# Kernel tuning notes

Hardware: AMD Instinct MI355X
Metric: run time of the kernel (lower is better)

## Reference

```python
import jax, jax.numpy as jnp
import numpy as np

B, S, D = 4, 4096, 64

def setup_inputs() -> dict:
    key = jax.random.key(0)
    ks = jax.random.split(key, 6)
    mk = lambda k: jax.random.normal(k, (B, S, D), dtype=jnp.float32)
    return {
        "q_re": mk(ks[0]), "q_im": mk(ks[1]),
        "k_re": mk(ks[2]), "k_im": mk(ks[3]),
        "v_re": mk(ks[4]), "v_im": mk(ks[5]),
    }

def reference(q_re, q_im, k_re, k_im, v_re, v_im):
    # Complex QK^T (no conjugate, matching torch.bmm on complex tensors):
    # (qr + i qi)(kr + i ki)^T -> re = qr kr^T - qi ki^T ; im = qr ki^T + qi kr^T
    d_k = q_re.shape[-1]
    scale = 1.0 / jnp.sqrt(jnp.asarray(d_k, dtype=q_re.dtype))
    s_re = (jnp.einsum('bqd,bkd->bqk', q_re, k_re)
            - jnp.einsum('bqd,bkd->bqk', q_im, k_im)) * scale
    s_im = (jnp.einsum('bqd,bkd->bqk', q_re, k_im)
            + jnp.einsum('bqd,bkd->bqk', q_im, k_re)) * scale
    # softmax over |scores| along key axis; weights are real (imag part is 0)
    w = jax.nn.softmax(jnp.sqrt(s_re * s_re + s_im * s_im), axis=-1)  # [B,S,S]
    # CVDropout is identity in eval mode. Output = real_weights @ complex_values
    o_re = jnp.einsum('bqk,bkd->bqd', w, v_re)
    o_im = jnp.einsum('bqk,bkd->bqd', w, v_im)
    return jnp.stack([o_re, o_im], axis=0)  # [2, B, S, D] (real, imag)
```

## Files before the change

kernel.cpp:

```cpp
#include <hip/hip_runtime.h>
#include <stdint.h>

#define B_    4
#define S_    4096
#define D_    64
#define QBLK  128
#define NELEM (B_ * S_ * D_)
#define BS_   (B_ * S_)

typedef __attribute__((ext_vector_type(8))) short bf16x8;
typedef __attribute__((ext_vector_type(4))) short bf16x4;
typedef __attribute__((ext_vector_type(4))) float f32x4;
typedef __attribute__((ext_vector_type(4))) int   i32x4;
typedef __attribute__((ext_vector_type(4))) unsigned u32x4;
typedef __attribute__((ext_vector_type(4))) _Float16 f16x4;

#define MFMA(a, b, c) __builtin_amdgcn_mfma_f32_16x16x32_bf16(a, b, c, 0, 0, 0)
#define VMWAIT(n) asm volatile("s_waitcnt vmcnt(" #n ")" ::: "memory")
#define BARRIER() do { asm volatile("" ::: "memory"); __builtin_amdgcn_s_barrier(); asm volatile("" ::: "memory"); } while (0)
#define LGKM_FENCE() do { asm volatile("s_waitcnt lgkmcnt(0)" ::: "memory"); __builtin_amdgcn_sched_barrier(0); } while (0)

__device__ __forceinline__ short f2bf(float x) {
    unsigned u = __builtin_bit_cast(unsigned, x);
    u += 0x7FFFu + ((u >> 16) & 1u);
    return (short)(u >> 16);
}

__device__ __forceinline__ unsigned cvtpk(float lo, float hi) {
    unsigned r;
    asm("v_cvt_pk_bf16_f32 %0, %1, %2" : "=v"(r) : "v"(lo), "v"(hi));
    return r;
}

__device__ __forceinline__ void async16(const short* g, short* l) {
    __builtin_amdgcn_global_load_lds(
        (const __attribute__((address_space(1))) unsigned int*)g,
        (__attribute__((address_space(3))) unsigned int*)l, 16, 0, 0);
}

__global__ __launch_bounds__(256)
void prepass_kernel(const float* __restrict__ q_re, const float* __restrict__ q_im,
                    const float* __restrict__ k_re, const float* __restrict__ k_im,
                    const float* __restrict__ v_re, const float* __restrict__ v_im,
                    short* __restrict__ ws) {
    const int bidx = blockIdx.x;
    const int tid  = threadIdx.x;
    if (bidx < 4096) {
        const int idx = bidx * 256 + tid;
        const int tn  = idx >> 18;
        const int e4  = idx & ((1 << 18) - 1);
        const float* s = (tn == 0 ? q_re : tn == 1 ? q_im : tn == 2 ? k_re : k_im)
                         + (size_t)e4 * 4;
        const float sc = (tn < 2) ? 0.125f : 1.0f;
        f32x4 x = *(const f32x4*)s;
        bf16x4 v;
#pragma unroll
        for (int c = 0; c < 4; ++c) v[c] = f2bf(x[c] * sc);
        *(bf16x4*)(ws + (size_t)tn * NELEM + (size_t)e4 * 4) = v;
    } else {
        __shared__ short tile[64][72];
        const int tb   = bidx - 4096;
        const int sb   = tb & 63;
        const int b    = (tb >> 6) & 3;
        const int comp = tb >> 8;
        const float* src = comp ? v_im : v_re;
        short* dst = ws + (size_t)(4 + comp) * NELEM;
#pragma unroll
        for (int i = 0; i < 4; ++i) {
            const int slot = i * 256 + tid;
            const int s  = slot >> 4;
            const int d4 = slot & 15;
            f32x4 x = *(const f32x4*)(src + (((size_t)b * S_) + sb * 64 + s) * D_ + d4 * 4);
#pragma unroll
            for (int c = 0; c < 4; ++c) tile[d4 * 4 + c][s] = f2bf(x[c]);
        }
        __syncthreads();
#pragma unroll
        for (int i = 0; i < 2; ++i) {
            const int slot = i * 256 + tid;
            const int d = slot >> 3;
            const int m = slot & 7;
            const int a = m >> 2, hh = m & 3;
            bf16x8 v;
#pragma unroll
            for (int j = 0; j < 8; ++j)
                v[j] = tile[d][a * 32 + hh * 4 + ((j >> 2) << 4) + (j & 3)];
            *(bf16x8*)(dst + ((size_t)b * 64 + d) * S_ + sb * 64 + m * 8) = v;
        }
    }
}

template<int SPLIT, typename OT>
__global__ __launch_bounds__(256, 2)
void cv_attn_main(const short* __restrict__ wsb,
                  float* __restrict__ out,
                  OT* __restrict__ opart,
                  float* __restrict__ ml)
{
    __shared__ __align__(16) short smem[2 * 8192];

    const int tid  = threadIdx.x;
    const int lane = tid & 63;
    const int wv   = tid >> 6;
    const int l15  = lane & 15;
    const int h    = lane >> 4;

    int bid = blockIdx.x;
    const int nwg = B_ * 32 * SPLIT;
    bid = (bid & 7) * (nwg >> 3) + (bid >> 3);
    const int qb = bid & 31;
    const int sp = (bid >> 5) % SPLIT;
    const int b  = bid / (32 * SPLIT);

    const short* qr = wsb;
    const short* qi = wsb + (size_t)NELEM;
    const short* kr = wsb + 2 * (size_t)NELEM;
    const short* ki = wsb + 3 * (size_t)NELEM;
    const short* vT = wsb + 4 * (size_t)NELEM;

    const short* p0 = smem + l15 * 64 + ((h ^ (l15 & 7)) << 3);
    const short* p1 = smem + l15 * 64 + (((h ^ 4) ^ (l15 & 7)) << 3);

    bf16x8 fqr[2][2], fqi[2][2];
#pragma unroll
    for (int g = 0; g < 2; ++g) {
        const int qrow = qb * QBLK + wv * 32 + g * 16 + l15;
        const size_t qoff = ((size_t)b * S_ + qrow) * D_;
#pragma unroll
        for (int dh = 0; dh < 2; ++dh) {
            fqr[g][dh] = *(const bf16x8*)(qr + qoff + dh * 32 + h * 8);
            fqi[g][dh] = *(const bf16x8*)(qi + qoff + dh * 32 + h * 8);
        }
    }

    f32x4 o_re[2][4], o_im[2][4];
#pragma unroll
    for (int g = 0; g < 2; ++g)
#pragma unroll
        for (int i = 0; i < 4; ++i) {
            o_re[g][i] = (f32x4){0.f, 0.f, 0.f, 0.f};
            o_im[g][i] = (f32x4){0.f, 0.f, 0.f, 0.f};
        }
    float l_run[2] = {0.f, 0.f};
    const float L2E = 1.44269504088896f;
    const float NM  = -16.0f * L2E;

    const int srcg = (lane & 7) ^ (lane >> 3);
    const int kRow = wv * 8 + (lane >> 3);
    constexpr int TPB = (S_ / 32) / SPLIT;

    auto stage = [&](int t, int DST) {
        const int kb = (sp * TPB + t) * 32;
        const size_t koff = ((size_t)b * S_ + kb + kRow) * 64 + (srcg << 3);
        async16(kr + koff, smem + DST + wv * 512);
        async16(ki + koff, smem + DST + 2048 + wv * 512);
#pragma unroll
        for (int i = 0; i < 2; ++i) {
            const int d = (wv + 4 * i) * 8 + (lane >> 3);
            const short* src = vT + ((srcg >> 2) ? (size_t)NELEM : (size_t)0)
                               + ((size_t)b * 64 + d) * S_ + kb + (srcg & 3) * 8;
            async16(src, smem + DST + 4096 + wv * 512 + i * 2048);
        }
    };

    auto body = [&](int t, int CUR, int OTH) {
        VMWAIT(0);
        LGKM_FENCE();
        BARRIER();
        if (t + 1 < TPB) stage(t + 1, OTH);

        f32x4 s_re[2][2], s_im[2][2];
#pragma unroll
        for (int g = 0; g < 2; ++g)
#pragma unroll
            for (int c = 0; c < 2; ++c) {
                s_re[g][c] = (f32x4){0.f, 0.f, 0.f, 0.f};
                s_im[g][c] = (f32x4){0.f, 0.f, 0.f, 0.f};
            }
        __builtin_amdgcn_s_setprio(1);
#pragma unroll
        for (int c = 0; c < 2; ++c) {
            bf16x8 a0 = *(const bf16x8*)(p0 + CUR + c * 1024);
            bf16x8 a1 = *(const bf16x8*)(p1 + CUR + c * 1024);
            bf16x8 b0 = *(const bf16x8*)(p0 + CUR + 2048 + c * 1024);
            bf16x8 b1 = *(const bf16x8*)(p1 + CUR + 2048 + c * 1024);
#pragma unroll
            for (int g = 0; g < 2; ++g) {
                i32x4 n0 = __builtin_bit_cast(i32x4, fqi[g][0]) ^ (int)0x80008000;
                i32x4 n1 = __builtin_bit_cast(i32x4, fqi[g][1]) ^ (int)0x80008000;
                bf16x8 fn0 = __builtin_bit_cast(bf16x8, n0);
                bf16x8 fn1 = __builtin_bit_cast(bf16x8, n1);
                s_re[g][c] = MFMA(a0, fqr[g][0], s_re[g][c]);
                s_re[g][c] = MFMA(a1, fqr[g][1], s_re[g][c]);
                s_re[g][c] = MFMA(b0, fn0,       s_re[g][c]);
                s_re[g][c] = MFMA(b1, fn1,       s_re[g][c]);
                s_im[g][c] = MFMA(b0, fqr[g][0], s_im[g][c]);
                s_im[g][c] = MFMA(b1, fqr[g][1], s_im[g][c]);
                s_im[g][c] = MFMA(a0, fqi[g][0], s_im[g][c]);
                s_im[g][c] = MFMA(a1, fqi[g][1], s_im[g][c]);
            }
        }
        __builtin_amdgcn_s_setprio(0);

        bf16x8 pb[2];
#pragma unroll
        for (int g = 0; g < 2; ++g) {
#pragma unroll
            for (int c = 0; c < 2; ++c) {
                f32x4 gm = s_re[g][c] * s_re[g][c] + s_im[g][c] * s_im[g][c];
#pragma unroll
                for (int r = 0; r < 4; ++r) {
                    const float mg = __builtin_amdgcn_sqrtf(gm[r]);
                    s_im[g][c][r] = __builtin_amdgcn_exp2f(__builtin_fmaf(mg, L2E, NM));
                }
            }
            f32x4 ps = s_im[g][0] + s_im[g][1];
            l_run[g] += (ps[0] + ps[1]) + (ps[2] + ps[3]);
            u32x4 w;
            w[0] = cvtpk(s_im[g][0][0], s_im[g][0][1]);
            w[1] = cvtpk(s_im[g][0][2], s_im[g][0][3]);
            w[2] = cvtpk(s_im[g][1][0], s_im[g][1][1]);
            w[3] = cvtpk(s_im[g][1][2], s_im[g][1][3]);
            pb[g] = __builtin_bit_cast(bf16x8, w);
        }

        __builtin_amdgcn_s_setprio(1);
#pragma unroll
        for (int dc = 0; dc < 4; ++dc) {
            bf16x8 av = *(const bf16x8*)(p0 + CUR + 4096 + dc * 1024);
            bf16x8 ai = *(const bf16x8*)(p1 + CUR + 4096 + dc * 1024);
#pragma unroll
            for (int g = 0; g < 2; ++g) {
                o_re[g][dc] = MFMA(av, pb[g], o_re[g][dc]);
                o_im[g][dc] = MFMA(ai, pb[g], o_im[g][dc]);
            }
        }
        __builtin_amdgcn_s_setprio(0);
    };

    stage(0, 0);
    for (int tt = 0; tt < TPB; tt += 2) {
        body(tt,     0,    8192);
        body(tt + 1, 8192, 0);
    }

    float inv[2];
    float lt[2];
#pragma unroll
    for (int g = 0; g < 2; ++g) {
        float l = l_run[g];
        l += __shfl_xor(l, 16);
        l += __shfl_xor(l, 32);
        lt[g]  = l;
        inv[g] = 1.0f / l;
    }

    float* ol = (float*)smem;

    OT* dst_re;
    OT* dst_im;
    if constexpr (SPLIT == 1) {
        dst_re = (OT*)out + ((size_t)b * S_ + qb * QBLK) * D_;
        dst_im = dst_re + (size_t)NELEM;
    } else {
        const size_t qo = ((size_t)b * S_ + qb * QBLK) * D_;
        dst_re = opart + ((size_t)sp * 2 + 0) * NELEM + qo;
        dst_im = opart + ((size_t)sp * 2 + 1) * NELEM + qo;
    }

    auto store_comp = [&](const f32x4 (&oc)[2][4], OT* og) {
#pragma unroll
        for (int half = 0; half < 2; ++half) {
            __syncthreads();
            if ((wv >> 1) == half) {
                const int wl = wv & 1;
#pragma unroll
                for (int g = 0; g < 2; ++g)
#pragma unroll
                    for (int dc = 0; dc < 4; ++dc)
#pragma unroll
                        for (int r = 0; r < 4; ++r)
                            ol[(wl * 32 + g * 16 + l15) * 65 + dc * 16 + h * 4 + r]
                                = oc[g][dc][r] * inv[g];
            }
            __syncthreads();
#pragma unroll
            for (int i = 0; i < 4; ++i) {
                const int slot = i * 256 + tid;
                const int row  = slot >> 4;
                const int c4   = slot & 15;
                f32x4 v;
#pragma unroll
                for (int j = 0; j < 4; ++j) v[j] = ol[row * 65 + c4 * 4 + j];
                if constexpr (sizeof(OT) == 4) {
                    *(f32x4*)((float*)og + (size_t)(half * 64 + row) * D_ + c4 * 4) = v;
                } else {
                    f16x4 hv;
#pragma unroll
                    for (int j = 0; j < 4; ++j) hv[j] = (_Float16)v[j];
                    *(f16x4*)((_Float16*)og + (size_t)(half * 64 + row) * D_ + c4 * 4) = hv;
                }
            }
        }
    };
    store_comp(o_re, dst_re);
    store_comp(o_im, dst_im);

    if constexpr (SPLIT > 1) {
        if (lane < 16) {
#pragma unroll
            for (int g = 0; g < 2; ++g) {
                const int row = qb * QBLK + wv * 32 + g * 16 + lane;
                ml[(size_t)sp * BS_ + (size_t)b * S_ + row] = lt[g];
            }
        }
    }
}

template<int SPLIT, typename OT>
__global__ __launch_bounds__(256)
void cv_attn_combine(const OT* __restrict__ opart, const float* __restrict__ ml,
                     float* __restrict__ out) {
    const int idx  = blockIdx.x * 256 + threadIdx.x;
    const int d4   = idx & 15;
    const int rest = idx >> 4;
    const int row  = rest & (BS_ - 1);
    const int comp = rest >> 14;
    float W = 0.f;
    f32x4 acc = (f32x4){0.f, 0.f, 0.f, 0.f};
#pragma unroll
    for (int s = 0; s < SPLIT; ++s) {
        const float l = ml[(size_t)s * BS_ + row];
        W += l;
        const OT* op = opart + ((size_t)(s * 2 + comp)) * NELEM + (size_t)row * D_ + d4 * 4;
        f32x4 o;
        if constexpr (sizeof(OT) == 4) {
            o = *(const f32x4*)op;
        } else {
            f16x4 hv = *(const f16x4*)op;
#pragma unroll
            for (int j = 0; j < 4; ++j) o[j] = (float)hv[j];
        }
        acc += o * l;
    }
    acc *= (1.0f / W);
    *(f32x4*)(out + (size_t)comp * NELEM + (size_t)row * D_ + d4 * 4) = acc;
}

__global__ __launch_bounds__(256, 1)
void cv_attn_legacy(const float* __restrict__ q_re, const float* __restrict__ q_im,
                    const float* __restrict__ k_re, const float* __restrict__ k_im,
                    const float* __restrict__ v_re, const float* __restrict__ v_im,
                    float* __restrict__ out)
{
    __shared__ __align__(16) short smem[4 * 64 * D_];
    short* kr_s = smem;
    short* ki_s = smem + 4096;
    short* vr_s = smem + 8192;
    short* vi_s = smem + 12288;

    const int tid  = threadIdx.x;
    const int lane = tid & 63;
    const int wv   = tid >> 6;
    const int l15  = lane & 15;
    const int h    = lane >> 4;

    const int b  = blockIdx.x >> 6;
    const int qb = blockIdx.x & 63;
    const size_t boff = (size_t)b * S_ * D_;

    const int qrow = qb * 64 + wv * 16 + l15;
    const float* qrp = q_re + boff + (size_t)qrow * D_;
    const float* qip = q_im + boff + (size_t)qrow * D_;
    bf16x8 fqr[2], fqi[2], fqn[2];
#pragma unroll
    for (int dh = 0; dh < 2; ++dh) {
        const int d0 = dh * 32 + h * 8;
        f32x4 a0 = *(const f32x4*)(qrp + d0);
        f32x4 a1 = *(const f32x4*)(qrp + d0 + 4);
        f32x4 b0 = *(const f32x4*)(qip + d0);
        f32x4 b1 = *(const f32x4*)(qip + d0 + 4);
#pragma unroll
        for (int j = 0; j < 4; ++j) {
            fqr[dh][j] = f2bf(a0[j]); fqr[dh][j + 4] = f2bf(a1[j]);
            fqi[dh][j] = f2bf(b0[j]); fqi[dh][j + 4] = f2bf(b1[j]);
            fqn[dh][j] = f2bf(-b0[j]); fqn[dh][j + 4] = f2bf(-b1[j]);
        }
    }

    f32x4 o_re[4], o_im[4];
#pragma unroll
    for (int i = 0; i < 4; ++i) {
        o_re[i] = (f32x4){0.f, 0.f, 0.f, 0.f};
        o_im[i] = (f32x4){0.f, 0.f, 0.f, 0.f};
    }
    float m_run = -1e30f, l_run = 0.f;
    const float SC = 0.125f * 1.44269504088896f;

    for (int t = 0; t < S_ / 64; ++t) {
        const int kb = t * 64;
#pragma unroll
        for (int a = 0; a < 2; ++a) {
            const float* src = (a ? k_im : k_re) + boff;
            short* dst = a ? ki_s : kr_s;
#pragma unroll
            for (int i = 0; i < 2; ++i) {
                const int slot = i * 256 + tid;
                const int row  = slot >> 3;
                const int cb   = slot & 7;
                const float* p = src + (size_t)(kb + row) * D_ + cb * 8;
                f32x4 x0 = *(const f32x4*)p;
                f32x4 x1 = *(const f32x4*)(p + 4);
                bf16x8 v;
#pragma unroll
                for (int j = 0; j < 4; ++j) { v[j] = f2bf(x0[j]); v[j + 4] = f2bf(x1[j]); }
                *(bf16x8*)(dst + row * 64 + ((cb ^ (row & 7)) << 3)) = v;
            }
        }
#pragma unroll
        for (int a = 0; a < 2; ++a) {
            const float* src = (a ? v_im : v_re) + boff;
            short* dst = a ? vi_s : vr_s;
#pragma unroll
            for (int i = 0; i < 4; ++i) {
                const int slot = i * 256 + tid;
                const int k  = slot >> 4;
                const int d4 = slot & 15;
                f32x4 x = *(const f32x4*)(src + (size_t)(kb + k) * D_ + d4 * 4);
#pragma unroll
                for (int c = 0; c < 4; ++c) {
                    const int d = d4 * 4 + c;
                    dst[d * 64 + (((k >> 2) ^ (d & 15)) << 2) + (k & 3)] = f2bf(x[c]);
                }
            }
        }
        __syncthreads();

        f32x4 s_re[4], s_im[4];
#pragma unroll
        for (int c = 0; c < 4; ++c) {
            s_re[c] = (f32x4){0.f, 0.f, 0.f, 0.f};
            s_im[c] = (f32x4){0.f, 0.f, 0.f, 0.f};
        }
#pragma unroll
        for (int c = 0; c < 4; ++c) {
            const int krow = c * 16 + l15;
#pragma unroll
            for (int dh = 0; dh < 2; ++dh) {
                const int u = ((dh * 4 + h) ^ (krow & 7)) << 3;
                bf16x8 fkr = *(const bf16x8*)(kr_s + krow * 64 + u);
                bf16x8 fki = *(const bf16x8*)(ki_s + krow * 64 + u);
                s_re[c] = MFMA(fkr, fqr[dh], s_re[c]);
                s_re[c] = MFMA(fki, fqn[dh], s_re[c]);
                s_im[c] = MFMA(fki, fqr[dh], s_im[c]);
                s_im[c] = MFMA(fkr, fqi[dh], s_im[c]);
            }
        }

        float pv[4][4];
        float tmax = 0.f;
#pragma unroll
        for (int c = 0; c < 4; ++c)
#pragma unroll
            for (int r = 0; r < 4; ++r) {
                const float re = s_re[c][r], im = s_im[c][r];
                const float mg = __builtin_amdgcn_sqrtf(re * re + im * im) * SC;
                pv[c][r] = mg;
                tmax = fmaxf(tmax, mg);
            }
        tmax = fmaxf(tmax, __shfl_xor(tmax, 16));
        tmax = fmaxf(tmax, __shfl_xor(tmax, 32));
        const float m_new = fmaxf(m_run, tmax);
        const float alpha = __builtin_amdgcn_exp2f(m_run - m_new);
        m_run = m_new;
        float psum = 0.f;
#pragma unroll
        for (int c = 0; c < 4; ++c)
#pragma unroll
            for (int r = 0; r < 4; ++r) {
                const float e = __builtin_amdgcn_exp2f(pv[c][r] - m_new);
                pv[c][r] = e;
                psum += e;
            }
        l_run = l_run * alpha + psum;
#pragma unroll
        for (int i = 0; i < 4; ++i) { o_re[i] *= alpha; o_im[i] *= alpha; }

        bf16x8 pb[2];
#pragma unroll
        for (int hf = 0; hf < 2; ++hf)
#pragma unroll
            for (int j = 0; j < 4; ++j) {
                pb[hf][j]     = f2bf(pv[hf * 2][j]);
                pb[hf][j + 4] = f2bf(pv[hf * 2 + 1][j]);
            }

#pragma unroll
        for (int hf = 0; hf < 2; ++hf) {
#pragma unroll
            for (int dc = 0; dc < 4; ++dc) {
                const int d  = dc * 16 + l15;
                const int s0 = (((hf * 8) + h)     ^ l15) << 2;
                const int s1 = (((hf * 8) + 4 + h) ^ l15) << 2;
                bf16x4 r0 = *(const bf16x4*)(vr_s + d * 64 + s0);
                bf16x4 r1 = *(const bf16x4*)(vr_s + d * 64 + s1);
                bf16x4 i0 = *(const bf16x4*)(vi_s + d * 64 + s0);
                bf16x4 i1 = *(const bf16x4*)(vi_s + d * 64 + s1);
                bf16x8 av, ai;
#pragma unroll
                for (int j = 0; j < 4; ++j) {
                    av[j] = r0[j]; av[j + 4] = r1[j];
                    ai[j] = i0[j]; ai[j + 4] = i1[j];
                }
                o_re[dc] = MFMA(av, pb[hf], o_re[dc]);
                o_im[dc] = MFMA(ai, pb[hf], o_im[dc]);
            }
        }
        __syncthreads();
    }

    float lt = l_run;
    lt += __shfl_xor(lt, 16);
    lt += __shfl_xor(lt, 32);
    const float inv = 1.0f / lt;

    float* ol = (float*)smem;
    auto store_comp = [&](const f32x4 (&oc)[4], float* og) {
#pragma unroll
        for (int dc = 0; dc < 4; ++dc)
#pragma unroll
            for (int r = 0; r < 4; ++r)
                ol[(wv * 16 + l15) * 65 + dc * 16 + h * 4 + r] = oc[dc][r] * inv;
        __syncthreads();
#pragma unroll
        for (int i = 0; i < 4; ++i) {
            const int slot = i * 256 + tid;
            const int row  = slot >> 4;
            const int c4   = slot & 15;
            f32x4 v;
#pragma unroll
            for (int j = 0; j < 4; ++j) v[j] = ol[row * 65 + c4 * 4 + j];
            *(f32x4*)(og + (size_t)row * D_ + c4 * 4) = v;
        }
        __syncthreads();
    };

    float* og0 = out + boff + (size_t)(qb * 64) * D_;
    store_comp(o_re, og0);
    store_comp(o_im, og0 + (size_t)B_ * S_ * D_);
}

extern "C" void kernel_launch(void* const* d_in, const int* in_sizes, int n_in,
                              void* d_out, int out_size, void* d_ws, size_t ws_size,
                              hipStream_t stream) {
    (void)in_sizes; (void)n_in; (void)out_size;
    const float* q_re = (const float*)d_in[0];
    const float* q_im = (const float*)d_in[1];
    const float* k_re = (const float*)d_in[2];
    const float* k_im = (const float*)d_in[3];
    const float* v_re = (const float*)d_in[4];
    const float* v_im = (const float*)d_in[5];
    float* out = (float*)d_out;

    const size_t bf_bytes = 6 * (size_t)NELEM * 2;
    const size_t need8f16 = bf_bytes + 8 * 2 * (size_t)NELEM * 2 + 8 * (size_t)BS_ * 4;
    const size_t need4f16 = bf_bytes + 4 * 2 * (size_t)NELEM * 2 + 4 * (size_t)BS_ * 4;

    if (ws_size >= bf_bytes) {
        short* wsb = (short*)d_ws;
        prepass_kernel<<<4608, 256, 0, stream>>>(q_re, q_im, k_re, k_im, v_re, v_im, wsb);
        char* extra = (char*)d_ws + bf_bytes;
        if (ws_size >= need8f16) {
            _Float16* opart = (_Float16*)extra;
            float* ml = (float*)(extra + 8 * 2 * (size_t)NELEM * 2);
            cv_attn_main<8, _Float16><<<B_ * 32 * 8, 256, 0, stream>>>(wsb, nullptr, opart, ml);
            cv_attn_combine<8, _Float16><<<2048, 256, 0, stream>>>(opart, ml, out);
        } else if (ws_size >= need4f16) {
            _Float16* opart = (_Float16*)extra;
            float* ml = (float*)(extra + 4 * 2 * (size_t)NELEM * 2);
            cv_attn_main<4, _Float16><<<B_ * 32 * 4, 256, 0, stream>>>(wsb, nullptr, opart, ml);
            cv_attn_combine<4, _Float16><<<2048, 256, 0, stream>>>(opart, ml, out);
        } else {
            cv_attn_main<1, float><<<B_ * 32, 256, 0, stream>>>(wsb, out, out, nullptr);
        }
    } else {
        cv_attn_legacy<<<B_ * 64, 256, 0, stream>>>(q_re, q_im, k_re, k_im, v_re, v_im, out);
    }
}
```

Before: 75.94 us.

## Load K/V tiles directly from global into registers instead of LDS double-buffering

Removes the async global-to-LDS double-buffered staging of K and V tiles, along with its waitcnt and barrier synchronization. Each wave now loads its K and V MFMA operands straight from global memory into registers every iteration. This drops the LDS traffic and block-wide barriers, but each of the four waves now fetches the same K/V data separately and the loads are no longer prefetched a tile ahead, so latency is exposed unless the L2 and compiler scheduling hide it. Shared memory shrinks to only the epilogue output buffer, which could raise occupancy.

```diff
diff --git a/kernel.cpp b/kernel.cpp
--- a/kernel.cpp
+++ b/kernel.cpp
@@ -16,9 +16,6 @@
 typedef __attribute__((ext_vector_type(4))) _Float16 f16x4;
 
 #define MFMA(a, b, c) __builtin_amdgcn_mfma_f32_16x16x32_bf16(a, b, c, 0, 0, 0)
-#define VMWAIT(n) asm volatile("s_waitcnt vmcnt(" #n ")" ::: "memory")
-#define BARRIER() do { asm volatile("" ::: "memory"); __builtin_amdgcn_s_barrier(); asm volatile("" ::: "memory"); } while (0)
-#define LGKM_FENCE() do { asm volatile("s_waitcnt lgkmcnt(0)" ::: "memory"); __builtin_amdgcn_sched_barrier(0); } while (0)
 
 __device__ __forceinline__ short f2bf(float x) {
     unsigned u = __builtin_bit_cast(unsigned, x);
@@ -30,12 +27,6 @@
     unsigned r;
     asm("v_cvt_pk_bf16_f32 %0, %1, %2" : "=v"(r) : "v"(lo), "v"(hi));
     return r;
-}
-
-__device__ __forceinline__ void async16(const short* g, short* l) {
-    __builtin_amdgcn_global_load_lds(
-        (const __attribute__((address_space(1))) unsigned int*)g,
-        (__attribute__((address_space(3))) unsigned int*)l, 16, 0, 0);
 }
 
 __global__ __launch_bounds__(256)
@@ -97,7 +88,7 @@
                   OT* __restrict__ opart,
                   float* __restrict__ ml)
 {
-    __shared__ __align__(16) short smem[2 * 8192];
+    __shared__ __align__(16) float ol[64 * 65];
 
     const int tid  = threadIdx.x;
     const int lane = tid & 63;
@@ -118,8 +109,10 @@
     const short* ki = wsb + 3 * (size_t)NELEM;
     const short* vT = wsb + 4 * (size_t)NELEM;
 
-    const short* p0 = smem + l15 * 64 + ((h ^ (l15 & 7)) << 3);
-    const short* p1 = smem + l15 * 64 + (((h ^ 4) ^ (l15 & 7)) << 3);
+    const short* krp = kr + ((size_t)b * S_ + l15) * 64 + h * 8;
+    const short* kip = ki + ((size_t)b * S_ + l15) * 64 + h * 8;
+    const short* vrp = vT + ((size_t)b * 64 + l15) * S_ + h * 8;
+    const short* vip = vrp + (size_t)NELEM;
 
     bf16x8 fqr[2][2], fqi[2][2];
 #pragma unroll
@@ -145,29 +138,27 @@
     const float L2E = 1.44269504088896f;
     const float NM  = -16.0f * L2E;
 
-    const int srcg = (lane & 7) ^ (lane >> 3);
-    const int kRow = wv * 8 + (lane >> 3);
     constexpr int TPB = (S_ / 32) / SPLIT;
-
-    auto stage = [&](int t, int DST) {
-        const int kb = (sp * TPB + t) * 32;
-        const size_t koff = ((size_t)b * S_ + kb + kRow) * 64 + (srcg << 3);
-        async16(kr + koff, smem + DST + wv * 512);
-        async16(ki + koff, smem + DST + 2048 + wv * 512);
-#pragma unroll
-        for (int i = 0; i < 2; ++i) {
-            const int d = (wv + 4 * i) * 8 + (lane >> 3);
-            const short* src = vT + ((srcg >> 2) ? (size_t)NELEM : (size_t)0)
-                               + ((size_t)b * 64 + d) * S_ + kb + (srcg & 3) * 8;
-            async16(src, smem + DST + 4096 + wv * 512 + i * 2048);
-        }
-    };
-
-    auto body = [&](int t, int CUR, int OTH) {
-        VMWAIT(0);
-        LGKM_FENCE();
-        BARRIER();
-        if (t + 1 < TPB) stage(t + 1, OTH);
+    const int kb0 = sp * TPB * 32;
+
+    for (int t = 0; t < TPB; ++t) {
+        const int kb = kb0 + t * 32;
+        const size_t kofs = (size_t)kb * 64;
+
+        bf16x8 ka[2][2], kc[2][2];
+#pragma unroll
+        for (int c = 0; c < 2; ++c)
+#pragma unroll
+            for (int dh = 0; dh < 2; ++dh) {
+                ka[c][dh] = *(const bf16x8*)(krp + kofs + c * 1024 + dh * 32);
+                kc[c][dh] = *(const bf16x8*)(kip + kofs + c * 1024 + dh * 32);
+            }
+        bf16x8 va[4], vb[4];
+#pragma unroll
+        for (int dc = 0; dc < 4; ++dc) {
+            va[dc] = *(const bf16x8*)(vrp + (size_t)dc * 16 * S_ + kb);
+            vb[dc] = *(const bf16x8*)(vip + (size_t)dc * 16 * S_ + kb);
+        }
 
         f32x4 s_re[2][2], s_im[2][2];
 #pragma unroll
@@ -179,27 +170,22 @@
             }
         __builtin_amdgcn_s_setprio(1);
 #pragma unroll
-        for (int c = 0; c < 2; ++c) {
-            bf16x8 a0 = *(const bf16x8*)(p0 + CUR + c * 1024);
-            bf16x8 a1 = *(const bf16x8*)(p1 + CUR + c * 1024);
-            bf16x8 b0 = *(const bf16x8*)(p0 + CUR + 2048 + c * 1024);
-            bf16x8 b1 = *(const bf16x8*)(p1 + CUR + 2048 + c * 1024);
+        for (int c = 0; c < 2; ++c)
 #pragma unroll
             for (int g = 0; g < 2; ++g) {
                 i32x4 n0 = __builtin_bit_cast(i32x4, fqi[g][0]) ^ (int)0x80008000;
                 i32x4 n1 = __builtin_bit_cast(i32x4, fqi[g][1]) ^ (int)0x80008000;
                 bf16x8 fn0 = __builtin_bit_cast(bf16x8, n0);
                 bf16x8 fn1 = __builtin_bit_cast(bf16x8, n1);
-                s_re[g][c] = MFMA(a0, fqr[g][0], s_re[g][c]);
-                s_re[g][c] = MFMA(a1, fqr[g][1], s_re[g][c]);
-                s_re[g][c] = MFMA(b0, fn0,       s_re[g][c]);
-                s_re[g][c] = MFMA(b1, fn1,       s_re[g][c]);
-                s_im[g][c] = MFMA(b0, fqr[g][0], s_im[g][c]);
-                s_im[g][c] = MFMA(b1, fqr[g][1], s_im[g][c]);
-                s_im[g][c] = MFMA(a0, fqi[g][0], s_im[g][c]);
-                s_im[g][c] = MFMA(a1, fqi[g][1], s_im[g][c]);
-            }
-        }
+                s_re[g][c] = MFMA(ka[c][0], fqr[g][0], s_re[g][c]);
+                s_re[g][c] = MFMA(ka[c][1], fqr[g][1], s_re[g][c]);
+                s_re[g][c] = MFMA(kc[c][0], fn0,       s_re[g][c]);
+                s_re[g][c] = MFMA(kc[c][1], fn1,       s_re[g][c]);
+                s_im[g][c] = MFMA(kc[c][0], fqr[g][0], s_im[g][c]);
+                s_im[g][c] = MFMA(kc[c][1], fqr[g][1], s_im[g][c]);
+                s_im[g][c] = MFMA(ka[c][0], fqi[g][0], s_im[g][c]);
+                s_im[g][c] = MFMA(ka[c][1], fqi[g][1], s_im[g][c]);
+            }
         __builtin_amdgcn_s_setprio(0);
 
         bf16x8 pb[2];
@@ -226,22 +212,13 @@
 
         __builtin_amdgcn_s_setprio(1);
 #pragma unroll
-        for (int dc = 0; dc < 4; ++dc) {
-            bf16x8 av = *(const bf16x8*)(p0 + CUR + 4096 + dc * 1024);
-            bf16x8 ai = *(const bf16x8*)(p1 + CUR + 4096 + dc * 1024);
+        for (int dc = 0; dc < 4; ++dc)
 #pragma unroll
             for (int g = 0; g < 2; ++g) {
-                o_re[g][dc] = MFMA(av, pb[g], o_re[g][dc]);
-                o_im[g][dc] = MFMA(ai, pb[g], o_im[g][dc]);
-            }
-        }
+                o_re[g][dc] = MFMA(va[dc], pb[g], o_re[g][dc]);
+                o_im[g][dc] = MFMA(vb[dc], pb[g], o_im[g][dc]);
+            }
         __builtin_amdgcn_s_setprio(0);
-    };
-
-    stage(0, 0);
-    for (int tt = 0; tt < TPB; tt += 2) {
-        body(tt,     0,    8192);
-        body(tt + 1, 8192, 0);
     }
 
     float inv[2];
@@ -254,8 +231,6 @@
         lt[g]  = l;
         inv[g] = 1.0f / l;
     }
-
-    float* ol = (float*)smem;
 
     OT* dst_re;
     OT* dst_im;
```

Result: slower. 144.1 us (+89.8%).
